# Kernel tuning notes

Hardware: AMD Instinct MI355X
Metric: run time of the kernel (lower is better)

Reference implementation:

```python
import jax, jax.numpy as jnp
import numpy as np

N = 50000
E = 1600000
D = 128
NUM_BOND_FEATS = 3
BOND_VOCAB = 5
BN_EPS = 1e-5


def setup_inputs() -> dict:
    key = jax.random.key(0)
    ks = jax.random.split(key, 12)
    x = jax.random.normal(ks[0], (N, D), dtype=jnp.float32)
    edge_attr = jax.random.randint(ks[1], (E, NUM_BOND_FEATS), 0, BOND_VOCAB, dtype=jnp.int64)
    src = jax.random.randint(ks[2], (E,), 0, N, dtype=jnp.int64)
    dst = jax.random.randint(ks[3], (E,), 0, N, dtype=jnp.int64)
    # BondEncoder: one embedding table per bond feature
    bond_emb = jax.random.normal(ks[4], (NUM_BOND_FEATS, BOND_VOCAB, D), dtype=jnp.float32) * 0.02
    # GIN eps parameter (init 0)
    eps = jnp.zeros((), dtype=jnp.float32)
    # MLP: Linear(D,D) -> BatchNorm1d(D) -> ReLU -> Linear(D,D)
    s = 1.0 / np.sqrt(D)
    W1 = jax.random.uniform(ks[5], (D, D), minval=-s, maxval=s, dtype=jnp.float32)
    b1 = jax.random.uniform(ks[6], (D,), minval=-s, maxval=s, dtype=jnp.float32)
    gamma = jnp.ones((D,), dtype=jnp.float32)
    beta = jnp.zeros((D,), dtype=jnp.float32)
    W2 = jax.random.uniform(ks[7], (D, D), minval=-s, maxval=s, dtype=jnp.float32)
    b2 = jax.random.uniform(ks[8], (D,), minval=-s, maxval=s, dtype=jnp.float32)
    return {"x": x, "edge_attr": edge_attr, "src": src, "dst": dst,
            "bond_emb": bond_emb, "eps": eps, "W1": W1, "b1": b1,
            "gamma": gamma, "beta": beta, "W2": W2, "b2": b2}


def reference(x, edge_attr, src, dst, bond_emb, eps, W1, b1, gamma, beta, W2, b2):
    # BondEncoder: sum of per-feature categorical embeddings -> [E, D]
    edge_embedding = bond_emb[jnp.arange(NUM_BOND_FEATS)[None, :], edge_attr].sum(axis=1)
    # copy_u gather + add edge emb + ReLU (per-edge messages)
    m = jax.nn.relu(x[src] + edge_embedding)            # [E, D]
    # scatter-sum aggregation to destination nodes
    agg = jax.ops.segment_sum(m, dst, num_segments=N)   # [N, D]
    h = (1.0 + eps) * x + agg
    # MLP: Linear -> BatchNorm (batch stats, training mode) -> ReLU -> Linear
    h1 = h @ W1 + b1
    mean = jnp.mean(h1, axis=0)
    var = jnp.var(h1, axis=0)
    hn = (h1 - mean) * jax.lax.rsqrt(var + BN_EPS) * gamma + beta
    out = jax.nn.relu(hn) @ W2 + b2
    return out
```

## Files before the change

kernel.cpp:

```cpp
#include <hip/hip_runtime.h>
#include <hip/hip_bf16.h>

#define NN 50000
#define NE 1600000
#define D 128
#define NB 784
#define CAP 2560
#define EPT 4
#define NROW 50048
#define LDWU 68
#define BINTH 400384

typedef __attribute__((ext_vector_type(8))) short bf16x8;
typedef __attribute__((ext_vector_type(4))) float f32x4;

__device__ __forceinline__ unsigned short f2bf(float f) {
  unsigned u = __float_as_uint(f);
  u += 0x7FFFu + ((u >> 16) & 1u);
  return (unsigned short)(u >> 16);
}
__device__ __forceinline__ float bf2f(unsigned short h) {
  return __uint_as_float((unsigned)h << 16);
}

__global__ __launch_bounds__(1024) void k_bin(const float* __restrict__ x,
                                              const float* __restrict__ bemb,
                                              const float* __restrict__ W1,
                                              const float* __restrict__ W2,
                                              const int* __restrict__ dst,
                                              const int* __restrict__ src,
                                              const int* __restrict__ ea,
                                              int* __restrict__ bucketCnt,
                                              unsigned* __restrict__ staging,
                                              ushort* __restrict__ xh,
                                              ushort* __restrict__ cth,
                                              ushort* __restrict__ w1t,
                                              ushort* __restrict__ w2t) {
  __shared__ int lcnt[NB], gbase[NB], lcur[NB];
  const int tid = threadIdx.x;
  const int gid = blockIdx.x * 1024 + tid;
  for (int i = tid; i < NB; i += 1024) { lcnt[i] = 0; lcur[i] = 0; }

  if (gid < 125 * D) {
    const int c = gid >> 7;
    const int k = gid & 127;
    const float v = bemb[(c / 25) * D + k] + bemb[(5 + (c % 25) / 5) * D + k] +
                    bemb[(10 + c % 5) * D + k];
    cth[gid] = f2bf(v);
  }
  if (gid < 2 * 16384) {
    const int m = gid >> 14;
    const int idx = gid & 16383;
    const int c = idx >> 7;
    const int k = idx & 127;
    const float w = m ? W2[k * 128 + c] : W1[k * 128 + c];
    (m ? w2t : w1t)[idx] = f2bf(w);
  }
  for (int i = gid; i < NN * D / 4; i += BINTH) {
    const float4 v = *(const float4*)(x + i * 4);
    ushort4 h;
    h.x = f2bf(v.x); h.y = f2bf(v.y); h.z = f2bf(v.z); h.w = f2bf(v.w);
    *(ushort4*)(xh + i * 4) = h;
  }

  const int e0 = gid * EPT;
  const bool act = (e0 < NE);

  int d[EPT];
  unsigned rec[EPT];
  if (act) {
    const int4 dv = *(const int4*)(dst + e0);
    const int4 sv = *(const int4*)(src + e0);
    const int4* ap = (const int4*)(ea + 3 * e0);
    int a[12];
#pragma unroll
    for (int q = 0; q < 3; ++q) {
      const int4 v = ap[q];
      a[4 * q + 0] = v.x; a[4 * q + 1] = v.y; a[4 * q + 2] = v.z; a[4 * q + 3] = v.w;
    }
    d[0] = dv.x; d[1] = dv.y; d[2] = dv.z; d[3] = dv.w;
    rec[0] = sv.x; rec[1] = sv.y; rec[2] = sv.z; rec[3] = sv.w;
#pragma unroll
    for (int q = 0; q < EPT; ++q) {
      const unsigned cb = (unsigned)((a[3 * q] * 5 + a[3 * q + 1]) * 5 + a[3 * q + 2]);
      rec[q] |= (cb << 16) | ((unsigned)(d[q] & 63) << 23);
      atomicAdd(&lcnt[d[q] >> 6], 1);
    }
  }
  __syncthreads();
  for (int i = tid; i < NB; i += 1024)
    gbase[i] = atomicAdd(&bucketCnt[i], lcnt[i]);
  __syncthreads();
  if (act) {
#pragma unroll
    for (int q = 0; q < EPT; ++q) {
      const int b = d[q] >> 6;
      const int r = atomicAdd(&lcur[b], 1) + gbase[b];
      if (r < CAP) staging[(size_t)b * CAP + r] = rec[q];
    }
  }
}

__global__ __launch_bounds__(1024) void k_fine(const int* __restrict__ bucketCnt,
                                               unsigned* __restrict__ staging,
                                               int* __restrict__ beg,
                                               int* __restrict__ end) {
  __shared__ unsigned srec[CAP];
  __shared__ int hist[64], off[64], cur[64];
  const int tid = threadIdx.x;
  const int b = blockIdx.x;
  const int base = b * CAP;
  const int cnt = min(bucketCnt[b], CAP);

  if (tid < 64) { hist[tid] = 0; cur[tid] = 0; }
  for (int i = tid; i < cnt; i += 1024) srec[i] = staging[base + i];
  __syncthreads();
  for (int i = tid; i < cnt; i += 1024) atomicAdd(&hist[srec[i] >> 23], 1);
  __syncthreads();
  int v = 0;
  if (tid < 64) { v = hist[tid]; off[tid] = v; }
  __syncthreads();
  for (int s = 1; s < 64; s <<= 1) {
    int u = 0;
    if (tid < 64 && tid >= s) u = off[tid - s];
    __syncthreads();
    if (tid < 64) off[tid] += u;
    __syncthreads();
  }
  if (tid < 64) off[tid] -= v;
  __syncthreads();

  if (tid < 64) {
    const int n = b * 64 + tid;
    if (n < NN) {
      beg[n] = base + off[tid];
      end[n] = base + off[tid] + hist[tid];
    }
  }
  for (int i = tid; i < cnt; i += 1024) {
    const unsigned u = srec[i];
    const int node = u >> 23;
    const int r = atomicAdd(&cur[node], 1);
    staging[base + off[node] + r] = u & 0x7FFFFFu;
  }
}

__global__ __launch_bounds__(256, 4) void k_agg(const float* __restrict__ x,
                                                const ushort* __restrict__ xh,
                                                const ushort* __restrict__ cth,
                                                const float* __restrict__ epsp,
                                                const int* __restrict__ beg,
                                                const int* __restrict__ end,
                                                const unsigned* __restrict__ packed2,
                                                float* __restrict__ hbuf) {
  const int lane = threadIdx.x & 31;
  const int n = blockIdx.x * 8 + (threadIdx.x >> 5);
  const int col = lane << 2;

  const int jb = beg[n];
  const int je = end[n];
  float4 acc = make_float4(0.f, 0.f, 0.f, 0.f);

  for (int j0 = jb; j0 < je; j0 += 32) {
    const int rem = min(32, je - j0);
    const int pk = (j0 + lane < je) ? (int)packed2[j0 + lane] : 0;
    int t = 0;
    for (; t + 8 <= rem; t += 8) {
      unsigned p[8];
#pragma unroll
      for (int i = 0; i < 8; ++i) p[i] = (unsigned)__shfl(pk, t + i, 32);
      ushort4 xs[8];
#pragma unroll
      for (int i = 0; i < 8; ++i)
        xs[i] = *(const ushort4*)(xh + (size_t)(p[i] & 0xFFFF) * D + col);
#pragma unroll
      for (int i = 0; i < 8; ++i) {
        const ushort4 eh = *(const ushort4*)(cth + ((p[i] >> 16) & 0x7F) * D + col);
        acc.x += fmaxf(bf2f(xs[i].x) + bf2f(eh.x), 0.f);
        acc.y += fmaxf(bf2f(xs[i].y) + bf2f(eh.y), 0.f);
        acc.z += fmaxf(bf2f(xs[i].z) + bf2f(eh.z), 0.f);
        acc.w += fmaxf(bf2f(xs[i].w) + bf2f(eh.w), 0.f);
      }
    }
    for (; t < rem; ++t) {
      const unsigned p = (unsigned)__shfl(pk, t, 32);
      const ushort4 xv = *(const ushort4*)(xh + (size_t)(p & 0xFFFF) * D + col);
      const ushort4 eh = *(const ushort4*)(cth + ((p >> 16) & 0x7F) * D + col);
      acc.x += fmaxf(bf2f(xv.x) + bf2f(eh.x), 0.f);
      acc.y += fmaxf(bf2f(xv.y) + bf2f(eh.y), 0.f);
      acc.z += fmaxf(bf2f(xv.z) + bf2f(eh.z), 0.f);
      acc.w += fmaxf(bf2f(xv.w) + bf2f(eh.w), 0.f);
    }
  }

  const float eps1 = 1.0f + epsp[0];
  const float4 xv = *(const float4*)(x + (size_t)n * D + col);
  acc.x += eps1 * xv.x;
  acc.y += eps1 * xv.y;
  acc.z += eps1 * xv.z;
  acc.w += eps1 * xv.w;
  *(float4*)(hbuf + (size_t)n * D + col) = acc;
}

__global__ __launch_bounds__(256, 4) void k_mfma1(const float* __restrict__ hbuf,
                                                  const ushort* __restrict__ w1t,
                                                  const float* __restrict__ b1,
                                                  ushort* __restrict__ h1,
                                                  float* __restrict__ gsum,
                                                  float* __restrict__ gsumsq) {
  __shared__ uint sW[128 * LDWU];
  __shared__ float ssum[128], ssq[128];
  const int tid = threadIdx.x;
  {
    const uint* src = (const uint*)w1t;
    for (int i = tid; i < 8192; i += 256)
      sW[(i >> 6) * LDWU + (i & 63)] = src[i];
  }
  if (tid < 128) { ssum[tid] = 0.f; ssq[tid] = 0.f; }
  __syncthreads();

  const int l = tid & 63;
  const int la = l & 15;
  const int lb = l >> 4;
  const int rowbase = blockIdx.x * 64 + (tid >> 6) * 16;
  const int arow = rowbase + la;
  const float* ap = hbuf + (size_t)arow * 128 + lb * 8;

  f32x4 acc[8];
#pragma unroll
  for (int ct = 0; ct < 8; ++ct) acc[ct] = (f32x4){0.f, 0.f, 0.f, 0.f};

#pragma unroll
  for (int ks = 0; ks < 4; ++ks) {
    const float4 a0 = *(const float4*)(ap + ks * 32);
    const float4 a1 = *(const float4*)(ap + ks * 32 + 4);
    const float af[8] = {a0.x, a0.y, a0.z, a0.w, a1.x, a1.y, a1.z, a1.w};
    bf16x8 ahi, alo;
#pragma unroll
    for (int j = 0; j < 8; ++j) {
      const unsigned short hh = f2bf(af[j]);
      ahi[j] = (short)hh;
      alo[j] = (short)f2bf(af[j] - bf2f(hh));
    }
#pragma unroll
    for (int ct = 0; ct < 8; ++ct) {
      const int c = ct * 16 + la;
      const bf16x8 b = *(const bf16x8*)(sW + c * LDWU + ks * 16 + lb * 4);
      acc[ct] = __builtin_amdgcn_mfma_f32_16x16x32_bf16(ahi, b, acc[ct], 0, 0, 0);
      acc[ct] = __builtin_amdgcn_mfma_f32_16x16x32_bf16(alo, b, acc[ct], 0, 0, 0);
    }
  }

#pragma unroll
  for (int ct = 0; ct < 8; ++ct) {
    const int col = ct * 16 + la;
    const float bb = b1[col];
    float s = 0.f, q = 0.f;
#pragma unroll
    for (int r = 0; r < 4; ++r) {
      const int row = rowbase + lb * 4 + r;
      if (row < NN) {
        const float v = acc[ct][r] + bb;
        const unsigned short hq = f2bf(v);
        h1[(size_t)row * 128 + col] = hq;
        const float vq = bf2f(hq);
        s += vq;
        q += vq * vq;
      }
    }
    s += __shfl_xor(s, 16, 64); q += __shfl_xor(q, 16, 64);
    s += __shfl_xor(s, 32, 64); q += __shfl_xor(q, 32, 64);
    if (lb == 0) { atomicAdd(&ssum[col], s); atomicAdd(&ssq[col], q); }
  }
  __syncthreads();
  if (tid < 128) {
    atomicAdd(&gsum[tid], ssum[tid]);
    atomicAdd(&gsumsq[tid], ssq[tid]);
  }
}

__global__ __launch_bounds__(256, 4) void k_mfma2(const ushort* __restrict__ h1,
                                                  const ushort* __restrict__ w2t,
                                                  const float* __restrict__ gsum,
                                                  const float* __restrict__ gsq,
                                                  const float* __restrict__ gamma,
                                                  const float* __restrict__ beta,
                                                  const float* __restrict__ b2,
                                                  float* __restrict__ out) {
  __shared__ uint sW[128 * LDWU];
  __shared__ float bnA[128], bnB[128];
  const int tid = threadIdx.x;
  {
    const uint* src = (const uint*)w2t;
    for (int i = tid; i < 8192; i += 256)
      sW[(i >> 6) * LDWU + (i & 63)] = src[i];
  }
  if (tid < 128) {
    const float invN = 1.0f / (float)NN;
    const float m = gsum[tid] * invN;
    const float A = gamma[tid] * rsqrtf(gsq[tid] * invN - m * m + 1e-5f);
    bnA[tid] = A;
    bnB[tid] = beta[tid] - m * A;
  }
  __syncthreads();

  const int l = tid & 63;
  const int la = l & 15;
  const int lb = l >> 4;
  const int rowbase = blockIdx.x * 64 + (tid >> 6) * 16;
  const int arow = rowbase + la;
  const ushort* ap = h1 + (size_t)arow * 128 + lb * 8;

  f32x4 acc[8];
#pragma unroll
  for (int ct = 0; ct < 8; ++ct) acc[ct] = (f32x4){0.f, 0.f, 0.f, 0.f};

#pragma unroll
  for (int ks = 0; ks < 4; ++ks) {
    const int k0 = ks * 32 + lb * 8;
    const bf16x8 araw = *(const bf16x8*)(ap + ks * 32);
    const float4 cA0 = *(const float4*)(bnA + k0);
    const float4 cA1 = *(const float4*)(bnA + k0 + 4);
    const float4 cB0 = *(const float4*)(bnB + k0);
    const float4 cB1 = *(const float4*)(bnB + k0 + 4);
    const float af[8] = {
        fmaxf(fmaf(bf2f((unsigned short)araw[0]), cA0.x, cB0.x), 0.f),
        fmaxf(fmaf(bf2f((unsigned short)araw[1]), cA0.y, cB0.y), 0.f),
        fmaxf(fmaf(bf2f((unsigned short)araw[2]), cA0.z, cB0.z), 0.f),
        fmaxf(fmaf(bf2f((unsigned short)araw[3]), cA0.w, cB0.w), 0.f),
        fmaxf(fmaf(bf2f((unsigned short)araw[4]), cA1.x, cB1.x), 0.f),
        fmaxf(fmaf(bf2f((unsigned short)araw[5]), cA1.y, cB1.y), 0.f),
        fmaxf(fmaf(bf2f((unsigned short)araw[6]), cA1.z, cB1.z), 0.f),
        fmaxf(fmaf(bf2f((unsigned short)araw[7]), cA1.w, cB1.w), 0.f)};
    bf16x8 afr;
#pragma unroll
    for (int j = 0; j < 8; ++j) afr[j] = (short)f2bf(af[j]);
#pragma unroll
    for (int ct = 0; ct < 8; ++ct) {
      const int c = ct * 16 + la;
      const bf16x8 b = *(const bf16x8*)(sW + c * LDWU + ks * 16 + lb * 4);
      acc[ct] = __builtin_amdgcn_mfma_f32_16x16x32_bf16(afr, b, acc[ct], 0, 0, 0);
    }
  }

#pragma unroll
  for (int ct = 0; ct < 8; ++ct) {
    const int col = ct * 16 + la;
    const float bb = b2[col];
#pragma unroll
    for (int r = 0; r < 4; ++r) {
      const int row = rowbase + lb * 4 + r;
      if (row < NN) out[(size_t)row * 128 + col] = acc[ct][r] + bb;
    }
  }
}

extern "C" void kernel_launch(void* const* d_in, const int* in_sizes, int n_in,
                              void* d_out, int out_size, void* d_ws, size_t ws_size,
                              hipStream_t stream) {
  const float* x    = (const float*)d_in[0];
  const int* ea     = (const int*)d_in[1];
  const int* src    = (const int*)d_in[2];
  const int* dst    = (const int*)d_in[3];
  const float* bemb = (const float*)d_in[4];
  const float* epsp = (const float*)d_in[5];
  const float* W1   = (const float*)d_in[6];
  const float* b1   = (const float*)d_in[7];
  const float* gam  = (const float*)d_in[8];
  const float* bet  = (const float*)d_in[9];
  const float* W2   = (const float*)d_in[10];
  const float* b2   = (const float*)d_in[11];
  float* out = (float*)d_out;

  float* ws         = (float*)d_ws;
  float* hbuf       = ws;
  int* bucketCnt    = (int*)(ws + (size_t)NROW * D);
  float* gsum       = ws + (size_t)NROW * D + NB;
  float* gsumsq     = gsum + D;
  int* beg          = (int*)(gsumsq + D);
  int* endp         = beg + NN;
  ushort* cth       = (ushort*)(endp + NN);
  ushort* w1t       = cth + 125 * D;
  ushort* w2t       = w1t + 16384;
  ushort* xh        = w2t + 16384;
  unsigned* staging = (unsigned*)(xh + (size_t)NN * D);
  ushort* h1h       = (ushort*)(staging + (size_t)NB * CAP);

  hipMemsetAsync(hbuf + (size_t)NN * D, 0,
                 (size_t)((NROW - NN) * D + NB + 2 * D) * sizeof(float), stream);

  k_bin<<<(NE / EPT + 1023) / 1024, 1024, 0, stream>>>(
      x, bemb, W1, W2, dst, src, ea, bucketCnt, staging, xh, cth, w1t, w2t);
  k_fine<<<NB, 1024, 0, stream>>>(bucketCnt, staging, beg, endp);
  k_agg<<<NN / 8, 256, 0, stream>>>(x, xh, cth, epsp, beg, endp, staging, hbuf);
  k_mfma1<<<NROW / 64, 256, 0, stream>>>(hbuf, w1t, b1, h1h, gsum, gsumsq);
  k_mfma2<<<NROW / 64, 256, 0, stream>>>(h1h, w2t, gsum, gsumsq, gam, bet, b2, out);
}
```

Measured before the change: 268.8 us.

## Fuse per-bucket fine sort with neighbor aggregation using LDS-resident sorted edges

Merges the fine counting-sort kernel and the aggregation kernel into one kernel per 64-node bucket. The sorted edge records stay in shared memory and drive the gather directly, so the sorted-edge write-back to global memory, the beg/end arrays and one kernel launch all go away. In exchange there are only 784 blocks of 1024 threads, each handling 2 nodes per wavefront-half, with twice the LDS per block. That lowers occupancy and parallelism for the latency-bound gather compared with the old 6250-block aggregation launch.

After: 274.6 us. 1.02x slower.

```diff
diff --git a/kernel.cpp b/kernel.cpp
--- a/kernel.cpp
+++ b/kernel.cpp
@@ -101,11 +101,15 @@
   }
 }
 
-__global__ __launch_bounds__(1024) void k_fine(const int* __restrict__ bucketCnt,
-                                               unsigned* __restrict__ staging,
-                                               int* __restrict__ beg,
-                                               int* __restrict__ end) {
+__global__ __launch_bounds__(1024) void k_fagg(const int* __restrict__ bucketCnt,
+                                               const unsigned* __restrict__ staging,
+                                               const float* __restrict__ x,
+                                               const ushort* __restrict__ xh,
+                                               const ushort* __restrict__ cth,
+                                               const float* __restrict__ epsp,
+                                               float* __restrict__ hbuf) {
   __shared__ unsigned srec[CAP];
+  __shared__ unsigned ssort[CAP];
   __shared__ int hist[64], off[64], cur[64];
   const int tid = threadIdx.x;
   const int b = blockIdx.x;
@@ -129,77 +133,68 @@
   }
   if (tid < 64) off[tid] -= v;
   __syncthreads();
-
-  if (tid < 64) {
-    const int n = b * 64 + tid;
-    if (n < NN) {
-      beg[n] = base + off[tid];
-      end[n] = base + off[tid] + hist[tid];
-    }
-  }
   for (int i = tid; i < cnt; i += 1024) {
     const unsigned u = srec[i];
     const int node = u >> 23;
     const int r = atomicAdd(&cur[node], 1);
-    staging[base + off[node] + r] = u & 0x7FFFFFu;
-  }
-}
-
-__global__ __launch_bounds__(256, 4) void k_agg(const float* __restrict__ x,
-                                                const ushort* __restrict__ xh,
-                                                const ushort* __restrict__ cth,
-                                                const float* __restrict__ epsp,
-                                                const int* __restrict__ beg,
-                                                const int* __restrict__ end,
-                                                const unsigned* __restrict__ packed2,
-                                                float* __restrict__ hbuf) {
-  const int lane = threadIdx.x & 31;
-  const int n = blockIdx.x * 8 + (threadIdx.x >> 5);
+    ssort[off[node] + r] = u & 0x7FFFFFu;
+  }
+  __syncthreads();
+
+  const int lane = tid & 31;
+  const int w = tid >> 5;
+  const float eps1 = 1.0f + epsp[0];
   const int col = lane << 2;
 
-  const int jb = beg[n];
-  const int je = end[n];
-  float4 acc = make_float4(0.f, 0.f, 0.f, 0.f);
-
-  for (int j0 = jb; j0 < je; j0 += 32) {
-    const int rem = min(32, je - j0);
-    const int pk = (j0 + lane < je) ? (int)packed2[j0 + lane] : 0;
-    int t = 0;
-    for (; t + 8 <= rem; t += 8) {
-      unsigned p[8];
-#pragma unroll
-      for (int i = 0; i < 8; ++i) p[i] = (unsigned)__shfl(pk, t + i, 32);
-      ushort4 xs[8];
-#pragma unroll
-      for (int i = 0; i < 8; ++i)
-        xs[i] = *(const ushort4*)(xh + (size_t)(p[i] & 0xFFFF) * D + col);
-#pragma unroll
-      for (int i = 0; i < 8; ++i) {
-        const ushort4 eh = *(const ushort4*)(cth + ((p[i] >> 16) & 0x7F) * D + col);
-        acc.x += fmaxf(bf2f(xs[i].x) + bf2f(eh.x), 0.f);
-        acc.y += fmaxf(bf2f(xs[i].y) + bf2f(eh.y), 0.f);
-        acc.z += fmaxf(bf2f(xs[i].z) + bf2f(eh.z), 0.f);
-        acc.w += fmaxf(bf2f(xs[i].w) + bf2f(eh.w), 0.f);
+#pragma unroll
+  for (int pass = 0; pass < 2; ++pass) {
+    const int localn = w + pass * 32;
+    const int n = b * 64 + localn;
+    const int jb = off[localn];
+    const int je = jb + hist[localn];
+    float4 acc = make_float4(0.f, 0.f, 0.f, 0.f);
+
+    for (int j0 = jb; j0 < je; j0 += 32) {
+      const int rem = min(32, je - j0);
+      const int pk = (j0 + lane < je) ? (int)ssort[j0 + lane] : 0;
+      int t = 0;
+      for (; t + 8 <= rem; t += 8) {
+        unsigned p[8];
+#pragma unroll
+        for (int i = 0; i < 8; ++i) p[i] = (unsigned)__shfl(pk, t + i, 32);
+        ushort4 xs[8];
+#pragma unroll
+        for (int i = 0; i < 8; ++i)
+          xs[i] = *(const ushort4*)(xh + (size_t)(p[i] & 0xFFFF) * D + col);
+#pragma unroll
+        for (int i = 0; i < 8; ++i) {
+          const ushort4 eh = *(const ushort4*)(cth + ((p[i] >> 16) & 0x7F) * D + col);
+          acc.x += fmaxf(bf2f(xs[i].x) + bf2f(eh.x), 0.f);
+          acc.y += fmaxf(bf2f(xs[i].y) + bf2f(eh.y), 0.f);
+          acc.z += fmaxf(bf2f(xs[i].z) + bf2f(eh.z), 0.f);
+          acc.w += fmaxf(bf2f(xs[i].w) + bf2f(eh.w), 0.f);
+        }
       }
-    }
-    for (; t < rem; ++t) {
-      const unsigned p = (unsigned)__shfl(pk, t, 32);
-      const ushort4 xv = *(const ushort4*)(xh + (size_t)(p & 0xFFFF) * D + col);
-      const ushort4 eh = *(const ushort4*)(cth + ((p >> 16) & 0x7F) * D + col);
-      acc.x += fmaxf(bf2f(xv.x) + bf2f(eh.x), 0.f);
-      acc.y += fmaxf(bf2f(xv.y) + bf2f(eh.y), 0.f);
-      acc.z += fmaxf(bf2f(xv.z) + bf2f(eh.z), 0.f);
-      acc.w += fmaxf(bf2f(xv.w) + bf2f(eh.w), 0.f);
-    }
-  }
-
-  const float eps1 = 1.0f + epsp[0];
-  const float4 xv = *(const float4*)(x + (size_t)n * D + col);
-  acc.x += eps1 * xv.x;
-  acc.y += eps1 * xv.y;
-  acc.z += eps1 * xv.z;
-  acc.w += eps1 * xv.w;
-  *(float4*)(hbuf + (size_t)n * D + col) = acc;
+      for (; t < rem; ++t) {
+        const unsigned p = (unsigned)__shfl(pk, t, 32);
+        const ushort4 xv = *(const ushort4*)(xh + (size_t)(p & 0xFFFF) * D + col);
+        const ushort4 eh = *(const ushort4*)(cth + ((p >> 16) & 0x7F) * D + col);
+        acc.x += fmaxf(bf2f(xv.x) + bf2f(eh.x), 0.f);
+        acc.y += fmaxf(bf2f(xv.y) + bf2f(eh.y), 0.f);
+        acc.z += fmaxf(bf2f(xv.z) + bf2f(eh.z), 0.f);
+        acc.w += fmaxf(bf2f(xv.w) + bf2f(eh.w), 0.f);
+      }
+    }
+
+    if (n < NN) {
+      const float4 xv = *(const float4*)(x + (size_t)n * D + col);
+      acc.x += eps1 * xv.x;
+      acc.y += eps1 * xv.y;
+      acc.z += eps1 * xv.z;
+      acc.w += eps1 * xv.w;
+      *(float4*)(hbuf + (size_t)n * D + col) = acc;
+    }
+  }
 }
 
 __global__ __launch_bounds__(256, 4) void k_mfma1(const float* __restrict__ hbuf,
@@ -377,9 +372,7 @@
   int* bucketCnt    = (int*)(ws + (size_t)NROW * D);
   float* gsum       = ws + (size_t)NROW * D + NB;
   float* gsumsq     = gsum + D;
-  int* beg          = (int*)(gsumsq + D);
-  int* endp         = beg + NN;
-  ushort* cth       = (ushort*)(endp + NN);
+  ushort* cth       = (ushort*)(gsumsq + D);
   ushort* w1t       = cth + 125 * D;
   ushort* w2t       = w1t + 16384;
   ushort* xh        = w2t + 16384;
@@ -391,8 +384,7 @@
 
   k_bin<<<(NE / EPT + 1023) / 1024, 1024, 0, stream>>>(
       x, bemb, W1, W2, dst, src, ea, bucketCnt, staging, xh, cth, w1t, w2t);
-  k_fine<<<NB, 1024, 0, stream>>>(bucketCnt, staging, beg, endp);
-  k_agg<<<NN / 8, 256, 0, stream>>>(x, xh, cth, epsp, beg, endp, staging, hbuf);
+  k_fagg<<<NB, 1024, 0, stream>>>(bucketCnt, staging, x, xh, cth, epsp, hbuf);
   k_mfma1<<<NROW / 64, 256, 0, stream>>>(hbuf, w1t, b1, h1h, gsum, gsumsq);
   k_mfma2<<<NROW / 64, 256, 0, stream>>>(h1h, w2t, gsum, gsumsq, gam, bet, b2, out);
 }
```
